# Optimization experiments

Measured on AMD Instinct MI355X. Metric: run time of the kernel, lower is better.

The kernel has to match this reference:

```python
import jax, jax.numpy as jnp
import numpy as np

B, CIN, COUT, H, W = 16, 128, 128, 64, 64
K1, K2, DIL = 3, 3, 1
PAD0 = DIL * (K1 - 1) // 2
PAD1 = DIL * (K2 - 1) // 2
L = H * W


def setup_inputs() -> dict:
    key = jax.random.key(0)
    k1, k2, k3, k4, k5 = jax.random.split(key, 5)
    x = jax.random.normal(k1, (B, CIN, H, W), dtype=jnp.float32)
    # binary per-pixel mask over kernel taps, broadcast over batch*channels
    mask = (jax.random.uniform(k2, (1, K1 * K2, L)) < 0.5).astype(jnp.float32)
    fan_in = CIN * K1 * K2
    bound = 1.0 / np.sqrt(fan_in)
    weight = jax.random.uniform(k3, (COUT, CIN, K1, K2), jnp.float32, -bound, bound)
    mask_weight = jax.random.uniform(k4, (COUT, K1, K2), jnp.float32, -bound, bound)
    bias = jax.random.uniform(k5, (COUT,), jnp.float32, -bound, bound)
    return {"x": x, "mask": mask, "weight": weight, "mask_weight": mask_weight, "bias": bias}


def reference(x, mask, weight, mask_weight, bias):
    # im2col: [B, CIN*K1*K2, H, W]; channel ordering (cin, k1, k2) matches torch unfold
    patches = jax.lax.conv_general_dilated_patches(
        x, (K1, K2), (1, 1), [(PAD0, PAD0), (PAD1, PAD1)], rhs_dilation=(DIL, DIL))
    p = patches.reshape(B, CIN, K1 * K2, L)
    p = p * mask[:, None, :, :]          # mask [1, K, L] broadcasts over B and CIN
    p = p.reshape(B, CIN * K1 * K2, L)
    out = jnp.einsum('ok,bkl->bol', weight.reshape(COUT, -1), p)
    out = out + bias[None, :, None]
    out = out + jnp.einsum('ok,mkl->mol', mask_weight.reshape(COUT, -1), mask)
    return out.reshape(B, COUT, H, W)
```

## Files before the change

### kernel.cpp

```cpp
#include <hip/hip_runtime.h>
#include <stdint.h>

#define B_    16
#define CIN_  128
#define COUT_ 128
#define H_    64
#define W_    64
#define L_    4096
#define KK_   1152
#define PW_   66
#define PPIX_ (PW_ * PW_)

typedef unsigned short u16;
typedef __bf16 bf16x8 __attribute__((ext_vector_type(8)));
typedef float  floatx4 __attribute__((ext_vector_type(4)));
typedef uint32_t u32x4 __attribute__((ext_vector_type(4)));

typedef const __attribute__((address_space(1))) uint32_t* gptr_t;
typedef __attribute__((address_space(3))) uint32_t*       lptr_t;

__device__ __forceinline__ void async_copy16(const void* g, void* l) {
    __builtin_amdgcn_global_load_lds((gptr_t)g, (lptr_t)l, 16, 0, 0);
}

__device__ __forceinline__ u16 f2bf(float f) {
    uint32_t u = __builtin_bit_cast(uint32_t, f);
    uint32_t r = u + 0x7FFFu + ((u >> 16) & 1u);
    return (u16)(r >> 16);
}

__global__ void lmc_transpose_kernel(const float* __restrict__ x, u16* __restrict__ xTp) {
    __shared__ u16 tile[64][CIN_ + 8];
    const int b   = blockIdx.y;
    const int y   = blockIdx.x;
    const int tid = threadIdx.x;

    {
        const int c  = tid >> 1;
        const int x0 = (tid & 1) * 32;
        const float* src = x + ((size_t)b * CIN_ + c) * L_ + y * 64 + x0;
        #pragma unroll
        for (int j = 0; j < 32; j += 4) {
            float4 v = *reinterpret_cast<const float4*>(src + j);
            tile[x0 + j + 0][c] = f2bf(v.x);
            tile[x0 + j + 1][c] = f2bf(v.y);
            tile[x0 + j + 2][c] = f2bf(v.z);
            tile[x0 + j + 3][c] = f2bf(v.w);
        }
    }
    __syncthreads();

    u16* dstrow = xTp + ((size_t)(b * PW_ + (y + 1)) * PW_) * CIN_;
    {
        const int xx   = tid >> 2;
        const int cseg = (tid & 3) * 32;
        u16* dst = dstrow + (size_t)(xx + 1) * CIN_ + cseg;
        #pragma unroll
        for (int i = 0; i < 32; i += 8) {
            *reinterpret_cast<uint4*>(dst + i) =
                *reinterpret_cast<const uint4*>(&tile[xx][cseg + i]);
        }
    }
    const uint4 z = {0u, 0u, 0u, 0u};
    if (tid < 32) {
        const int pix = (tid >> 4) ? 65 : 0;
        *reinterpret_cast<uint4*>(dstrow + (size_t)pix * CIN_ + (tid & 15) * 8) = z;
    }
    if (y == 0 || y == 63) {
        u16* brow = xTp + ((size_t)(b * PW_ + (y == 0 ? 0 : 65)) * PW_) * CIN_;
        for (int i = tid; i < (PW_ * CIN_) / 8; i += 256)
            reinterpret_cast<uint4*>(brow)[i] = z;
    }
}

__global__ void lmc_prep_kernel(const float* __restrict__ mask, const float* __restrict__ mw,
                                const float* __restrict__ bias, const float* __restrict__ w,
                                float* __restrict__ mb, u16* __restrict__ wb2) {
    const int bid = blockIdx.x, tid = threadIdx.x;
    if (bid < 128) {
        const int o = bid;
        float m[9];
        #pragma unroll
        for (int k = 0; k < 9; ++k) m[k] = mw[o * 9 + k];
        const float bs = bias[o];
        for (int l = tid; l < L_; l += 256) {
            float s = bs;
            #pragma unroll
            for (int k = 0; k < 9; ++k) s += m[k] * mask[k * L_ + l];
            mb[o * L_ + l] = s;
        }
    } else {
        const int base = (bid - 128) * 2304;
        #pragma unroll
        for (int i = 0; i < 9; ++i) {
            const int e = base + i * 256 + tid;
            const int k = e >> 14;
            const int rem = e & 16383;
            const int o = rem >> 7, c = rem & 127;
            wb2[e] = f2bf(w[(size_t)o * KK_ + c * 9 + k]);
        }
    }
}

__global__ __launch_bounds__(256, 2)
void lmc_gemm_kernel(const u16* __restrict__ xTp, const u16* __restrict__ wb2,
                     const float* __restrict__ mask, const float* __restrict__ mb,
                     float* __restrict__ out) {
    __shared__ u16 A_lds[128 * 128];
    __shared__ u16 B_lds[128 * 128];

    const int b    = blockIdx.y;
    const int l0   = blockIdx.x * 128;
    const int tid  = threadIdx.x;
    const int lane = tid & 63;
    const int wv   = tid >> 6;
    const int wm   = (wv >> 1) * 64;
    const int wn   = (wv & 1) * 64;
    const int lrow = lane & 15;
    const int quad = lane >> 4;

    uint32_t goffA[8];
    uint32_t goffB[8];
    #pragma unroll
    for (int s = 0; s < 8; ++s) {
        const int row = wv * 32 + s * 4 + (lane >> 4);
        const int cc  = (lane & 15) ^ (row & 7);
        goffA[s] = (uint32_t)(row * 256 + cc * 16);
        const int l  = l0 + row;
        const int yy = (l >> 6) + 1, xx = (l & 63) + 1;
        const int p  = (b * PW_ + yy) * PW_ + xx;
        goffB[s] = (uint32_t)(p * 256 + cc * 16);
    }

    uint64_t bits = 0;
    #pragma unroll
    for (int j = 0; j < 4; ++j) {
        const int l = l0 + wn + j * 16 + lrow;
        #pragma unroll
        for (int k = 0; k < 9; ++k)
            if (mask[k * L_ + l] != 0.0f) bits |= (1ull << (k * 4 + j));
    }

    floatx4 acc[4][4];
    #pragma unroll
    for (int i = 0; i < 4; ++i)
        #pragma unroll
        for (int j = 0; j < 4; ++j)
            acc[i][j] = (floatx4){0.f, 0.f, 0.f, 0.f};

    const char* xTp_c = (const char*)xTp;
    const char* wb2_c = (const char*)wb2;
    char* Ab = (char*)A_lds;
    char* Bb = (char*)B_lds;
    const int ldsbase = (wv * 8) * 1024;

    for (int k = 0; k < 9; ++k) {
        const int dy = k / 3 - 1;
        const int dx = k - (k / 3) * 3 - 1;
        const int tapoff = (dy * PW_ + dx) * 256;
        const int abase  = k * 32768;

        #pragma unroll
        for (int s = 0; s < 8; ++s)
            async_copy16(wb2_c + abase + goffA[s], Ab + ldsbase + s * 1024);
        #pragma unroll
        for (int s = 0; s < 8; ++s)
            async_copy16(xTp_c + (int)goffB[s] + tapoff, Bb + ldsbase + s * 1024);

        __syncthreads();

        uint32_t kp[4];
        #pragma unroll
        for (int j = 0; j < 4; ++j)
            kp[j] = 0u - (uint32_t)((bits >> (k * 4 + j)) & 1ull);

        #pragma unroll
        for (int ks = 0; ks < 4; ++ks) {
            const int sc = ((ks * 4 + quad) ^ (lrow & 7)) * 8;
            bf16x8 af[4], bfr[4];
            #pragma unroll
            for (int i = 0; i < 4; ++i)
                af[i] = *reinterpret_cast<const bf16x8*>(&A_lds[(wm + i * 16 + lrow) * 128 + sc]);
            #pragma unroll
            for (int j = 0; j < 4; ++j) {
                bf16x8 v = *reinterpret_cast<const bf16x8*>(&B_lds[(wn + j * 16 + lrow) * 128 + sc]);
                u32x4 t = __builtin_bit_cast(u32x4, v);
                t &= kp[j];
                bfr[j] = __builtin_bit_cast(bf16x8, t);
            }
            #pragma unroll
            for (int i = 0; i < 4; ++i)
                #pragma unroll
                for (int j = 0; j < 4; ++j)
                    acc[i][j] = __builtin_amdgcn_mfma_f32_16x16x32_bf16(af[i], bfr[j], acc[i][j], 0, 0, 0);
        }
        __syncthreads();
    }

    #pragma unroll
    for (int i = 0; i < 4; ++i) {
        #pragma unroll
        for (int j = 0; j < 4; ++j) {
            const int l = l0 + wn + j * 16 + lrow;
            #pragma unroll
            for (int r = 0; r < 4; ++r) {
                const int o = wm + i * 16 + quad * 4 + r;
                out[((size_t)b * COUT_ + o) * L_ + l] = acc[i][j][r] + mb[o * L_ + l];
            }
        }
    }
}

extern "C" void kernel_launch(void* const* d_in, const int* in_sizes, int n_in,
                              void* d_out, int out_size, void* d_ws, size_t ws_size,
                              hipStream_t stream) {
    const float* x      = (const float*)d_in[0];
    const float* mask   = (const float*)d_in[1];
    const float* weight = (const float*)d_in[2];
    const float* mw     = (const float*)d_in[3];
    const float* bias   = (const float*)d_in[4];
    float* out = (float*)d_out;

    char* ws = (char*)d_ws;
    u16*   xTp = (u16*)ws;
    u16*   wb2 = (u16*)(ws + 17842176);
    float* mb  = (float*)(ws + 17842176 + 294912);

    lmc_transpose_kernel<<<dim3(64, B_), 256, 0, stream>>>(x, xTp);
    lmc_prep_kernel<<<192, 256, 0, stream>>>(mask, mw, bias, weight, mb, wb2);
    lmc_gemm_kernel<<<dim3(L_ / 128, B_), 256, 0, stream>>>(xTp, wb2, mask, mb, out);
}
```

Before: 126.3 us.

## Double-buffer im2col tiles in LDS and load weights directly to registers

Weights are now read straight from global memory into registers per tap rather than staged through LDS, freeing LDS for a double-buffered activation tile. The next tap's activations are prefetched asynchronously while the current tap is computed, halving barriers. Block indices are remapped so consecutive workgroups are spread across batches/tiles for better cache locality. The direct global weight loads add latency in the inner loop and increase register pressure.

Measured after the change: 144.2 us. 14.2% more time.

```diff
diff --git a/kernel.cpp b/kernel.cpp
--- a/kernel.cpp
+++ b/kernel.cpp
@@ -106,11 +106,13 @@
 void lmc_gemm_kernel(const u16* __restrict__ xTp, const u16* __restrict__ wb2,
                      const float* __restrict__ mask, const float* __restrict__ mb,
                      float* __restrict__ out) {
-    __shared__ u16 A_lds[128 * 128];
-    __shared__ u16 B_lds[128 * 128];
-
-    const int b    = blockIdx.y;
-    const int l0   = blockIdx.x * 128;
+    __shared__ u16 B_lds[2 * 128 * 128];
+
+    const int flat    = blockIdx.y * gridDim.x + blockIdx.x;
+    const int logical = (flat & 7) * 64 + (flat >> 3);
+    const int b       = logical >> 5;
+    const int l0      = (logical & 31) * 128;
+
     const int tid  = threadIdx.x;
     const int lane = tid & 63;
     const int wv   = tid >> 6;
@@ -119,13 +121,11 @@
     const int lrow = lane & 15;
     const int quad = lane >> 4;
 
-    uint32_t goffA[8];
     uint32_t goffB[8];
     #pragma unroll
     for (int s = 0; s < 8; ++s) {
         const int row = wv * 32 + s * 4 + (lane >> 4);
         const int cc  = (lane & 15) ^ (row & 7);
-        goffA[s] = (uint32_t)(row * 256 + cc * 16);
         const int l  = l0 + row;
         const int yy = (l >> 6) + 1, xx = (l & 63) + 1;
         const int p  = (b * PW_ + yy) * PW_ + xx;
@@ -149,41 +149,52 @@
             acc[i][j] = (floatx4){0.f, 0.f, 0.f, 0.f};
 
     const char* xTp_c = (const char*)xTp;
-    const char* wb2_c = (const char*)wb2;
-    char* Ab = (char*)A_lds;
     char* Bb = (char*)B_lds;
     const int ldsbase = (wv * 8) * 1024;
 
-    for (int k = 0; k < 9; ++k) {
-        const int dy = k / 3 - 1;
-        const int dx = k - (k / 3) * 3 - 1;
-        const int tapoff = (dy * PW_ + dx) * 256;
-        const int abase  = k * 32768;
-
-        #pragma unroll
-        for (int s = 0; s < 8; ++s)
-            async_copy16(wb2_c + abase + goffA[s], Ab + ldsbase + s * 1024);
+    {
+        const int tapoff = (-PW_ - 1) * 256;
         #pragma unroll
         for (int s = 0; s < 8; ++s)
             async_copy16(xTp_c + (int)goffB[s] + tapoff, Bb + ldsbase + s * 1024);
-
-        __syncthreads();
+    }
+    __syncthreads();
+
+    for (int k = 0; k < 9; ++k) {
+        const int cur = (k & 1) * 32768;
+        if (k < 8) {
+            const int kn = k + 1;
+            const int dy = kn / 3 - 1;
+            const int dx = kn - (kn / 3) * 3 - 1;
+            const int tapoff = (dy * PW_ + dx) * 256;
+            char* Bnxt = Bb + (32768 - cur);
+            #pragma unroll
+            for (int s = 0; s < 8; ++s)
+                async_copy16(xTp_c + (int)goffB[s] + tapoff, Bnxt + ldsbase + s * 1024);
+        }
+
+        bf16x8 af[4][4];
+        const u16* wk = wb2 + k * 16384;
+        #pragma unroll
+        for (int i = 0; i < 4; ++i)
+            #pragma unroll
+            for (int ks = 0; ks < 4; ++ks)
+                af[i][ks] = *reinterpret_cast<const bf16x8*>(
+                    wk + (wm + i * 16 + lrow) * 128 + ks * 32 + quad * 8);
 
         uint32_t kp[4];
         #pragma unroll
         for (int j = 0; j < 4; ++j)
             kp[j] = 0u - (uint32_t)((bits >> (k * 4 + j)) & 1ull);
 
+        const u16* Bc = (const u16*)(Bb + cur);
         #pragma unroll
         for (int ks = 0; ks < 4; ++ks) {
             const int sc = ((ks * 4 + quad) ^ (lrow & 7)) * 8;
-            bf16x8 af[4], bfr[4];
-            #pragma unroll
-            for (int i = 0; i < 4; ++i)
-                af[i] = *reinterpret_cast<const bf16x8*>(&A_lds[(wm + i * 16 + lrow) * 128 + sc]);
+            bf16x8 bfr[4];
             #pragma unroll
             for (int j = 0; j < 4; ++j) {
-                bf16x8 v = *reinterpret_cast<const bf16x8*>(&B_lds[(wn + j * 16 + lrow) * 128 + sc]);
+                bf16x8 v = *reinterpret_cast<const bf16x8*>(&Bc[(wn + j * 16 + lrow) * 128 + sc]);
                 u32x4 t = __builtin_bit_cast(u32x4, v);
                 t &= kp[j];
                 bfr[j] = __builtin_bit_cast(bf16x8, t);
@@ -192,7 +203,7 @@
             for (int i = 0; i < 4; ++i)
                 #pragma unroll
                 for (int j = 0; j < 4; ++j)
-                    acc[i][j] = __builtin_amdgcn_mfma_f32_16x16x32_bf16(af[i], bfr[j], acc[i][j], 0, 0, 0);
+                    acc[i][j] = __builtin_amdgcn_mfma_f32_16x16x32_bf16(af[i][ks], bfr[j], acc[i][j], 0, 0, 0);
         }
         __syncthreads();
     }
```

## Stage input halo window once in LDS and stream weights from registers

Applied to the files above, without the earlier changes.

The GEMM kernel now loads a 6-row padded input window (396 pixels x 128 channels) into LDS once per block and reuses it for all nine taps by shifting pixel indices, instead of re-copying the B tile for every tap. Weight fragments are read straight from global memory into registers, with the next tap's fragments prefetched during the current MFMAs. This removes the per-tap LDS staging and barriers. Blocks grow to 512 threads covering 256 pixels, and a remapped block order groups neighbouring tiles. The cost is more register pressure from the prefetched fragments and about 100KB of LDS per block, which limits occupancy.

Measured after the change: 143.3 us. 1.14x slower.

```diff
diff --git a/kernel.cpp b/kernel.cpp
--- a/kernel.cpp
+++ b/kernel.cpp
@@ -102,43 +102,59 @@
     }
 }
 
-__global__ __launch_bounds__(256, 2)
+__global__ __launch_bounds__(512, 2)
 void lmc_gemm_kernel(const u16* __restrict__ xTp, const u16* __restrict__ wb2,
                      const float* __restrict__ mask, const float* __restrict__ mb,
                      float* __restrict__ out) {
-    __shared__ u16 A_lds[128 * 128];
-    __shared__ u16 B_lds[128 * 128];
-
-    const int b    = blockIdx.y;
-    const int l0   = blockIdx.x * 128;
+    __shared__ u16 W_lds[396 * 128];
+
+    const int flat    = blockIdx.x;
+    const int logical = (flat & 7) * 32 + (flat >> 3);
+    const int b       = logical >> 4;
+    const int lt      = logical & 15;
+    const int Y       = lt * 4;
+    const int l0      = lt * 256;
+
     const int tid  = threadIdx.x;
     const int lane = tid & 63;
     const int wv   = tid >> 6;
-    const int wm   = (wv >> 1) * 64;
-    const int wn   = (wv & 1) * 64;
+    const int wm   = (wv >> 2) * 64;
+    const int wn   = (wv & 3) * 64;
     const int lrow = lane & 15;
     const int quad = lane >> 4;
 
-    uint32_t goffA[8];
-    uint32_t goffB[8];
-    #pragma unroll
-    for (int s = 0; s < 8; ++s) {
-        const int row = wv * 32 + s * 4 + (lane >> 4);
-        const int cc  = (lane & 15) ^ (row & 7);
-        goffA[s] = (uint32_t)(row * 256 + cc * 16);
-        const int l  = l0 + row;
-        const int yy = (l >> 6) + 1, xx = (l & 63) + 1;
-        const int p  = (b * PW_ + yy) * PW_ + xx;
-        goffB[s] = (uint32_t)(p * 256 + cc * 16);
-    }
-
+    {
+        const char* xw = (const char*)xTp + ((size_t)(b * PW_ + Y) * PW_) * 256;
+        for (int t = wv; t < 99; t += 8) {
+            const int p    = t * 4 + quad;
+            const int srcc = lrow ^ (p & 7);
+            async_copy16(xw + (size_t)p * 256 + srcc * 16,
+                         (char*)W_lds + t * 1024);
+        }
+    }
+
+    int arow[4];
+    #pragma unroll
+    for (int i = 0; i < 4; ++i)
+        arow[i] = (wm + i * 16 + lrow) * 128 + quad * 8;
+
+    bf16x8 af[4][4];
+    #pragma unroll
+    for (int i = 0; i < 4; ++i)
+        #pragma unroll
+        for (int ks = 0; ks < 4; ++ks)
+            af[i][ks] = *reinterpret_cast<const bf16x8*>(wb2 + arow[i] + ks * 32);
+
+    int pix0[4];
     uint64_t bits = 0;
     #pragma unroll
     for (int j = 0; j < 4; ++j) {
-        const int l = l0 + wn + j * 16 + lrow;
+        const int ll = wn + j * 16 + lrow;
+        pix0[j] = ((ll >> 6) + 1) * 66 + (ll & 63) + 1;
+        const int lg = l0 + ll;
         #pragma unroll
         for (int k = 0; k < 9; ++k)
-            if (mask[k * L_ + l] != 0.0f) bits |= (1ull << (k * 4 + j));
+            if (mask[k * L_ + lg] != 0.0f) bits |= (1ull << (k * 4 + j));
     }
 
     floatx4 acc[4][4];
@@ -148,26 +164,14 @@
         for (int j = 0; j < 4; ++j)
             acc[i][j] = (floatx4){0.f, 0.f, 0.f, 0.f};
 
-    const char* xTp_c = (const char*)xTp;
-    const char* wb2_c = (const char*)wb2;
-    char* Ab = (char*)A_lds;
-    char* Bb = (char*)B_lds;
-    const int ldsbase = (wv * 8) * 1024;
+    __syncthreads();
 
     for (int k = 0; k < 9; ++k) {
         const int dy = k / 3 - 1;
         const int dx = k - (k / 3) * 3 - 1;
-        const int tapoff = (dy * PW_ + dx) * 256;
-        const int abase  = k * 32768;
-
-        #pragma unroll
-        for (int s = 0; s < 8; ++s)
-            async_copy16(wb2_c + abase + goffA[s], Ab + ldsbase + s * 1024);
-        #pragma unroll
-        for (int s = 0; s < 8; ++s)
-            async_copy16(xTp_c + (int)goffB[s] + tapoff, Bb + ldsbase + s * 1024);
-
-        __syncthreads();
+        const int sh = dy * 66 + dx;
+        const int kn = (k < 8) ? k + 1 : 8;
+        const u16* wkn = wb2 + kn * 16384;
 
         uint32_t kp[4];
         #pragma unroll
@@ -176,14 +180,12 @@
 
         #pragma unroll
         for (int ks = 0; ks < 4; ++ks) {
-            const int sc = ((ks * 4 + quad) ^ (lrow & 7)) * 8;
-            bf16x8 af[4], bfr[4];
-            #pragma unroll
-            for (int i = 0; i < 4; ++i)
-                af[i] = *reinterpret_cast<const bf16x8*>(&A_lds[(wm + i * 16 + lrow) * 128 + sc]);
+            bf16x8 bfr[4];
             #pragma unroll
             for (int j = 0; j < 4; ++j) {
-                bf16x8 v = *reinterpret_cast<const bf16x8*>(&B_lds[(wn + j * 16 + lrow) * 128 + sc]);
+                const int pix  = pix0[j] + sh;
+                const int slot = (ks * 4 + quad) ^ (pix & 7);
+                bf16x8 v = *reinterpret_cast<const bf16x8*>(&W_lds[pix * 128 + slot * 8]);
                 u32x4 t = __builtin_bit_cast(u32x4, v);
                 t &= kp[j];
                 bfr[j] = __builtin_bit_cast(bf16x8, t);
@@ -192,9 +194,11 @@
             for (int i = 0; i < 4; ++i)
                 #pragma unroll
                 for (int j = 0; j < 4; ++j)
-                    acc[i][j] = __builtin_amdgcn_mfma_f32_16x16x32_bf16(af[i], bfr[j], acc[i][j], 0, 0, 0);
-        }
-        __syncthreads();
+                    acc[i][j] = __builtin_amdgcn_mfma_f32_16x16x32_bf16(af[i][ks], bfr[j], acc[i][j], 0, 0, 0);
+            #pragma unroll
+            for (int i = 0; i < 4; ++i)
+                af[i][ks] = *reinterpret_cast<const bf16x8*>(wkn + arow[i] + ks * 32);
+        }
     }
 
     #pragma unroll
@@ -228,5 +232,5 @@
 
     lmc_transpose_kernel<<<dim3(64, B_), 256, 0, stream>>>(x, xTp);
     lmc_prep_kernel<<<192, 256, 0, stream>>>(mask, mw, bias, weight, mb, wb2);
-    lmc_gemm_kernel<<<dim3(L_ / 128, B_), 256, 0, stream>>>(xTp, wb2, mask, mb, out);
-}
+    lmc_gemm_kernel<<<dim3(256), 512, 0, stream>>>(xTp, wb2, mask, mb, out);
+}
```
